# Optimization experiments

Measured on AMD Instinct MI355X. Metric: run time of the kernel, lower is better.

The kernel has to match this reference:

```python
import jax, jax.numpy as jnp
import numpy as np

DIM = 512
HIDDEN = 1024
H2 = HIDDEN // 2
B = 384


def setup_inputs() -> dict:
    key = jax.random.key(0)
    ks = jax.random.split(key, 10)
    s_in = 1.0 / np.sqrt(DIM)
    s_h = 1.0 / np.sqrt(H2)
    return {
        "x_samples": jax.random.normal(ks[0], (B, DIM), dtype=jnp.float32),
        "y_samples": jax.random.normal(ks[1], (B, DIM), dtype=jnp.float32),
        "w1_mu": jax.random.uniform(ks[2], (DIM, H2), jnp.float32, -s_in, s_in),
        "b1_mu": jax.random.uniform(ks[3], (H2,), jnp.float32, -s_in, s_in),
        "w2_mu": jax.random.uniform(ks[4], (H2, DIM), jnp.float32, -s_h, s_h),
        "b2_mu": jax.random.uniform(ks[5], (DIM,), jnp.float32, -s_h, s_h),
        "w1_lv": jax.random.uniform(ks[6], (DIM, H2), jnp.float32, -s_in, s_in),
        "b1_lv": jax.random.uniform(ks[7], (H2,), jnp.float32, -s_in, s_in),
        "w2_lv": jax.random.uniform(ks[8], (H2, DIM), jnp.float32, -s_h, s_h),
        "b2_lv": jax.random.uniform(ks[9], (DIM,), jnp.float32, -s_h, s_h),
    }


def reference(x_samples, y_samples, w1_mu, b1_mu, w2_mu, b2_mu,
              w1_lv, b1_lv, w2_lv, b2_lv):
    batch_size = y_samples.shape[0]
    # p_mu / p_logvar MLPs
    mu = jax.nn.relu(x_samples @ w1_mu + b1_mu) @ w2_mu + b2_mu           # [B, D]
    logvar = jnp.tanh(jax.nn.relu(x_samples @ w1_lv + b1_lv) @ w2_lv + b2_lv)  # [B, D]
    inv_var = jnp.exp(-logvar)

    # positive log-likelihood per sample
    positive = (-(mu - y_samples) ** 2 * 0.5 * inv_var - logvar * 0.5).sum(-1)  # [B]

    # pairwise Gaussian log-likelihoods: all_probs[i, j] = log N(y_j; mu_i)
    diff = y_samples[None, :, :] - mu[:, None, :]                          # [B, B, D]
    all_probs = (-diff ** 2 * 0.5 * inv_var[:, None, :]
                 - logvar[:, None, :] * 0.5).sum(-1)                       # [B, B]

    # faithful to the torch broadcast: [B,B] + [B,B,1] -> [B,B,B]
    diag_mask = jnp.eye(batch_size, dtype=jnp.float32)[:, :, None] * -20.0  # [B, B, 1]
    scores = all_probs + diag_mask                                         # [B, B, B]
    negative = jax.scipy.special.logsumexp(scores, axis=0) - jnp.log(batch_size - 1.0)  # [B, B]

    upper = (positive - negative).mean()

    loglikeli = (-(mu - y_samples) ** 2 * inv_var - logvar).sum(1).mean(0)
    return loglikeli + jax.lax.stop_gradient(-loglikeli + upper)
```

## Files before the change

### kernel.cpp

```cpp
#include <hip/hip_runtime.h>
#include <math.h>

#define NROW 384
#define NCOL 512

#define HP_OFF   0
#define GP_OFF   1572864
#define M1P_OFF  3145728
#define M2P_OFF  3151872
#define M1_OFF   3158016
#define M2_OFF   3158528
#define PART_OFF 3159040
#define CNT_OFF  3159424
#define SLICE    196608

template<int NS>
__device__ __forceinline__ void gemm_block(
    const float* __restrict__ A, const float* __restrict__ bias1,
    const float* __restrict__ W, float* __restrict__ C,
    int m0, int n0, int ca)
{
    __shared__ __align__(16) float As[2][32][36];
    __shared__ __align__(16) float Bs[2][32][68];

    const int t  = threadIdx.x;
    const int tx = t & 15;
    const int ty = t >> 4;
    const int am0 = t >> 3;
    const int ak4 = (t & 7) * 4;
    const int bk  = t >> 4;
    const int bn4 = (t & 15) * 4;

    float4 a_raw[2][NS];
    float4 b_raw[4];
    float4 bias_raw;

    auto load_it = [&](int k0) {
        #pragma unroll
        for (int p = 0; p < 2; ++p) {
            const size_t aoff = (size_t)(m0 + am0 + p * 16) * NCOL + ca + k0 + ak4;
            #pragma unroll
            for (int s = 0; s < NS; ++s)
                a_raw[p][s] = *(const float4*)&A[(size_t)s * SLICE + aoff];
        }
        if (NS > 1) bias_raw = *(const float4*)&bias1[ca + k0 + ak4];
        #pragma unroll
        for (int q = 0; q < 4; ++q)
            b_raw[q] = *(const float4*)&W[(size_t)(ca + k0 + bk + 8 * q) * NCOL + n0 + bn4];
    };

    auto store_it = [&](int buf) {
        #pragma unroll
        for (int p = 0; p < 2; ++p) {
            float v[4];
            if (NS == 1) {
                *(float4*)v = a_raw[p][0];
            } else {
                float s0[4], s1[4], s2[4], s3[4], bb[4];
                *(float4*)s0 = a_raw[p][0]; *(float4*)s1 = a_raw[p][1];
                *(float4*)s2 = a_raw[p][2]; *(float4*)s3 = a_raw[p][3];
                *(float4*)bb = bias_raw;
                #pragma unroll
                for (int j = 0; j < 4; ++j)
                    v[j] = fmaxf(s0[j] + s1[j] + s2[j] + s3[j] + bb[j], 0.f);
            }
            #pragma unroll
            for (int j = 0; j < 4; ++j)
                As[buf][ak4 + j][am0 + p * 16] = v[j];
        }
        #pragma unroll
        for (int q = 0; q < 4; ++q)
            *(float4*)&Bs[buf][bk + 8 * q][bn4] = b_raw[q];
    };

    float acc[4][4] = {};

    load_it(0);
    store_it(0);
    __syncthreads();
    load_it(32);

    for (int it = 0; it < 4; ++it) {
        if (it < 3) {
            store_it((it + 1) & 1);
            if (it < 2) load_it((it + 2) * 32);
        }
        const int buf = it & 1;
        #pragma unroll
        for (int kk = 0; kk < 32; ++kk) {
            float av[4], bv[4];
            *(float4*)av = *(const float4*)&As[buf][kk][ty * 4];
            *(float4*)bv = *(const float4*)&Bs[buf][kk][tx * 4];
            #pragma unroll
            for (int i = 0; i < 4; ++i) {
                acc[i][0] += av[i] * bv[0];
                acc[i][1] += av[i] * bv[1];
                acc[i][2] += av[i] * bv[2];
                acc[i][3] += av[i] * bv[3];
            }
        }
        __syncthreads();
    }

    #pragma unroll
    for (int i = 0; i < 4; ++i)
        *(float4*)&C[(size_t)(m0 + ty * 4 + i) * NCOL + n0 + tx * 4] =
            make_float4(acc[i][0], acc[i][1], acc[i][2], acc[i][3]);
}

__global__ __launch_bounds__(128, 2) void k_layer1(
    const float* __restrict__ x,
    const float* __restrict__ w1mu, const float* __restrict__ w1lv,
    const float* __restrict__ y, float* __restrict__ ws)
{
    const int b = blockIdx.x;
    const int t = threadIdx.x;

    if (b >= 768) {
        const int sb = b - 768;
        const int c  = t * 4;
        float s1[4] = {0.f, 0.f, 0.f, 0.f};
        float s2[4] = {0.f, 0.f, 0.f, 0.f};
        #pragma unroll 4
        for (int r = 0; r < 32; ++r) {
            float v[4];
            *(float4*)v = *(const float4*)&y[(size_t)(sb * 32 + r) * NCOL + c];
            #pragma unroll
            for (int j = 0; j < 4; ++j) { s1[j] += v[j]; s2[j] += v[j] * v[j]; }
        }
        *(float4*)&ws[M1P_OFF + sb * NCOL + c] = make_float4(s1[0], s1[1], s1[2], s1[3]);
        *(float4*)&ws[M2P_OFF + sb * NCOL + c] = make_float4(s2[0], s2[1], s2[2], s2[3]);
        return;
    }

    const int sl   = b & 3;
    const int br   = (b >> 2) & 1;
    const int tile = b >> 3;
    const int mt   = tile >> 3;
    const int nt   = tile & 7;

    gemm_block<1>(x, nullptr, br ? w1lv : w1mu,
                  ws + HP_OFF + (size_t)(br * 4 + sl) * SLICE,
                  mt * 32, nt * 64, sl * 128);
}

__global__ __launch_bounds__(128, 2) void k_layer2(
    const float* __restrict__ b1mu, const float* __restrict__ b1lv,
    const float* __restrict__ w2mu, const float* __restrict__ w2lv,
    float* __restrict__ ws)
{
    const int b = blockIdx.x;
    const int t = threadIdx.x;

    if (b == 768) {
        if (t == 0) *(int*)(ws + CNT_OFF) = 0;
        const int c = t * 4;
        float s1[4] = {0.f, 0.f, 0.f, 0.f};
        float s2[4] = {0.f, 0.f, 0.f, 0.f};
        #pragma unroll
        for (int p = 0; p < 12; ++p) {
            float p1[4], p2[4];
            *(float4*)p1 = *(const float4*)&ws[M1P_OFF + p * NCOL + c];
            *(float4*)p2 = *(const float4*)&ws[M2P_OFF + p * NCOL + c];
            #pragma unroll
            for (int j = 0; j < 4; ++j) { s1[j] += p1[j]; s2[j] += p2[j]; }
        }
        *(float4*)&ws[M1_OFF + c] = make_float4(s1[0], s1[1], s1[2], s1[3]);
        *(float4*)&ws[M2_OFF + c] = make_float4(s2[0], s2[1], s2[2], s2[3]);
        return;
    }

    const int sl   = b & 3;
    const int br   = (b >> 2) & 1;
    const int tile = b >> 3;
    const int mt   = tile >> 3;
    const int nt   = tile & 7;

    gemm_block<4>(ws + HP_OFF + (size_t)(br * 4) * SLICE,
                  br ? b1lv : b1mu, br ? w2lv : w2mu,
                  ws + GP_OFF + (size_t)(br * 4 + sl) * SLICE,
                  mt * 32, nt * 64, sl * 128);
}

__global__ __launch_bounds__(256) void k_epilogue(
    const float* __restrict__ b2mu, const float* __restrict__ b2lv,
    const float* __restrict__ y, float* __restrict__ ws,
    float* __restrict__ out)
{
    __shared__ double wsum[4];
    __shared__ int is_last;

    const int t = threadIdx.x;
    const float inv_b = 1.0f / (float)NROW;

    const int e4   = blockIdx.x * 256 + t;
    const int col4 = e4 & 127;
    const size_t off = (size_t)e4 * 4;

    const float* gpm = ws + GP_OFF;
    const float* gpl = ws + GP_OFF + 4 * SLICE;

    float gm[4] = {0.f, 0.f, 0.f, 0.f};
    float gl[4] = {0.f, 0.f, 0.f, 0.f};
    #pragma unroll
    for (int s = 0; s < 4; ++s) {
        float a[4], c[4];
        *(float4*)a = *(const float4*)&gpm[(size_t)s * SLICE + off];
        *(float4*)c = *(const float4*)&gpl[(size_t)s * SLICE + off];
        #pragma unroll
        for (int j = 0; j < 4; ++j) { gm[j] += a[j]; gl[j] += c[j]; }
    }

    float yv[4], bm[4], bl[4], m1v[4], m2v[4];
    *(float4*)yv  = *(const float4*)&y[off];
    *(float4*)bm  = *(const float4*)&b2mu[col4 * 4];
    *(float4*)bl  = *(const float4*)&b2lv[col4 * 4];
    *(float4*)m1v = *(const float4*)&ws[M1_OFF + col4 * 4];
    *(float4*)m2v = *(const float4*)&ws[M2_OFF + col4 * 4];

    float tsum = 0.f;
    #pragma unroll
    for (int j = 0; j < 4; ++j) {
        const float m1 = m1v[j] * inv_b;
        const float m2 = m2v[j] * inv_b;
        const float mu = gm[j] + bm[j];
        const float lv = tanhf(gl[j] + bl[j]);
        const float iv = expf(-lv);
        tsum += iv * ((yv[j] * yv[j] - m2) + 2.f * mu * (m1 - yv[j]));
    }

    float s = tsum;
    #pragma unroll
    for (int o = 32; o > 0; o >>= 1) s += __shfl_down(s, o);
    if ((t & 63) == 0) wsum[t >> 6] = (double)s;
    __syncthreads();

    double* partials = (double*)(ws + PART_OFF);
    int* counter = (int*)(ws + CNT_OFF);
    if (t == 0) {
        partials[blockIdx.x] = wsum[0] + wsum[1] + wsum[2] + wsum[3];
        __threadfence();
        const int old = atomicAdd(counter, 1);
        is_last = (old == 191) ? 1 : 0;
    }
    __syncthreads();

    if (is_last && t < 64) {
        __threadfence();
        double v = partials[t] + partials[t + 64] + partials[t + 128];
        #pragma unroll
        for (int o = 32; o > 0; o >>= 1) v += __shfl_down(v, o);
        if (t == 0) {
            const double C0 = 5.381602146862063e-12;
            out[0] = (float)(-0.5 * v / (double)NROW - C0);
        }
    }
}

extern "C" void kernel_launch(void* const* d_in, const int* in_sizes, int n_in,
                              void* d_out, int out_size, void* d_ws, size_t ws_size,
                              hipStream_t stream) {
    const float* x    = (const float*)d_in[0];
    const float* y    = (const float*)d_in[1];
    const float* w1mu = (const float*)d_in[2];
    const float* b1mu = (const float*)d_in[3];
    const float* w2mu = (const float*)d_in[4];
    const float* b2mu = (const float*)d_in[5];
    const float* w1lv = (const float*)d_in[6];
    const float* b1lv = (const float*)d_in[7];
    const float* w2lv = (const float*)d_in[8];
    const float* b2lv = (const float*)d_in[9];
    float* out = (float*)d_out;
    float* ws  = (float*)d_ws;

    k_layer1<<<780, 128, 0, stream>>>(x, w1mu, w1lv, y, ws);
    k_layer2<<<769, 128, 0, stream>>>(b1mu, b1lv, w2mu, w2lv, ws);
    k_epilogue<<<192, 256, 0, stream>>>(b2mu, b2lv, y, ws, out);
}
```

Measured before the change: 112.2 us.

## Switch GEMMs to 64x128 tiles with 8-way split-K and 8x8 register blocking

Replaces the 32x64 double-buffered GEMM tile with a single-stage 64x128 tile that covers a 64-deep K chunk, using an 8x8 accumulator per thread and 8 split-K slices instead of 4. Layer-2 now sums 8 partial hidden slices while loading A, and the epilogue reduces 8 output partials. This raises arithmetic intensity per LDS load and halves the block count. In exchange it doubles the partial-sum workspace traffic, drops the load/compute overlap, and uses much more shared memory and registers per block, which may lower occupancy.

```diff
diff --git a/kernel.cpp b/kernel.cpp
--- a/kernel.cpp
+++ b/kernel.cpp
@@ -3,109 +3,94 @@
 
 #define NROW 384
 #define NCOL 512
+#define SLICE 196608
 
 #define HP_OFF   0
-#define GP_OFF   1572864
-#define M1P_OFF  3145728
-#define M2P_OFF  3151872
-#define M1_OFF   3158016
-#define M2_OFF   3158528
-#define PART_OFF 3159040
-#define CNT_OFF  3159424
-#define SLICE    196608
+#define GP_OFF   3145728
+#define M1P_OFF  6291456
+#define M2P_OFF  6297600
+#define M1_OFF   6303744
+#define M2_OFF   6304256
+#define PART_OFF 6304768
+#define CNT_OFF  6305152
 
 template<int NS>
-__device__ __forceinline__ void gemm_block(
+__device__ __forceinline__ void gemm64x128(
     const float* __restrict__ A, const float* __restrict__ bias1,
     const float* __restrict__ W, float* __restrict__ C,
     int m0, int n0, int ca)
 {
-    __shared__ __align__(16) float As[2][32][36];
-    __shared__ __align__(16) float Bs[2][32][68];
-
-    const int t  = threadIdx.x;
-    const int tx = t & 15;
-    const int ty = t >> 4;
-    const int am0 = t >> 3;
-    const int ak4 = (t & 7) * 4;
-    const int bk  = t >> 4;
-    const int bn4 = (t & 15) * 4;
-
-    float4 a_raw[2][NS];
-    float4 b_raw[4];
-    float4 bias_raw;
-
-    auto load_it = [&](int k0) {
-        #pragma unroll
-        for (int p = 0; p < 2; ++p) {
-            const size_t aoff = (size_t)(m0 + am0 + p * 16) * NCOL + ca + k0 + ak4;
-            #pragma unroll
-            for (int s = 0; s < NS; ++s)
-                a_raw[p][s] = *(const float4*)&A[(size_t)s * SLICE + aoff];
-        }
-        if (NS > 1) bias_raw = *(const float4*)&bias1[ca + k0 + ak4];
-        #pragma unroll
-        for (int q = 0; q < 4; ++q)
-            b_raw[q] = *(const float4*)&W[(size_t)(ca + k0 + bk + 8 * q) * NCOL + n0 + bn4];
-    };
-
-    auto store_it = [&](int buf) {
-        #pragma unroll
-        for (int p = 0; p < 2; ++p) {
+    __shared__ __align__(16) float As[64][68];
+    __shared__ __align__(16) float Bs[64][128];
+
+    const int t = threadIdx.x;
+
+    {
+        const int arow  = t & 63;
+        const int ahalf = t >> 6;
+        const float* ap = &A[(size_t)(m0 + arow) * NCOL + ca + ahalf * 32];
+        #pragma unroll
+        for (int g = 0; g < 8; ++g) {
             float v[4];
             if (NS == 1) {
-                *(float4*)v = a_raw[p][0];
+                *(float4*)v = *(const float4*)(ap + g * 4);
             } else {
-                float s0[4], s1[4], s2[4], s3[4], bb[4];
-                *(float4*)s0 = a_raw[p][0]; *(float4*)s1 = a_raw[p][1];
-                *(float4*)s2 = a_raw[p][2]; *(float4*)s3 = a_raw[p][3];
-                *(float4*)bb = bias_raw;
+                float s4[4] = {0.f, 0.f, 0.f, 0.f};
                 #pragma unroll
-                for (int j = 0; j < 4; ++j)
-                    v[j] = fmaxf(s0[j] + s1[j] + s2[j] + s3[j] + bb[j], 0.f);
+                for (int s = 0; s < NS; ++s) {
+                    float u[4];
+                    *(float4*)u = *(const float4*)(ap + (size_t)s * SLICE + g * 4);
+                    s4[0] += u[0]; s4[1] += u[1]; s4[2] += u[2]; s4[3] += u[3];
+                }
+                float bb[4];
+                *(float4*)bb = *(const float4*)&bias1[ca + ahalf * 32 + g * 4];
+                v[0] = fmaxf(s4[0] + bb[0], 0.f);
+                v[1] = fmaxf(s4[1] + bb[1], 0.f);
+                v[2] = fmaxf(s4[2] + bb[2], 0.f);
+                v[3] = fmaxf(s4[3] + bb[3], 0.f);
             }
+            const int k = ahalf * 32 + g * 4;
+            As[k + 0][arow] = v[0];
+            As[k + 1][arow] = v[1];
+            As[k + 2][arow] = v[2];
+            As[k + 3][arow] = v[3];
+        }
+    }
+
+    #pragma unroll
+    for (int i = 0; i < 16; ++i) {
+        const int f4 = t + i * 128;
+        const int kk = f4 >> 5;
+        const int c4 = (f4 & 31) * 4;
+        *(float4*)&Bs[kk][c4] =
+            *(const float4*)&W[(size_t)(ca + kk) * NCOL + n0 + c4];
+    }
+    __syncthreads();
+
+    const int ty = t >> 4, tx = t & 15;
+    float acc[8][8] = {};
+    #pragma unroll 16
+    for (int kk = 0; kk < 64; ++kk) {
+        float a[8], b[8];
+        *(float4*)&a[0] = *(const float4*)&As[kk][ty * 8];
+        *(float4*)&a[4] = *(const float4*)&As[kk][ty * 8 + 4];
+        *(float4*)&b[0] = *(const float4*)&Bs[kk][tx * 4];
+        *(float4*)&b[4] = *(const float4*)&Bs[kk][64 + tx * 4];
+        #pragma unroll
+        for (int i = 0; i < 8; ++i)
             #pragma unroll
-            for (int j = 0; j < 4; ++j)
-                As[buf][ak4 + j][am0 + p * 16] = v[j];
-        }
-        #pragma unroll
-        for (int q = 0; q < 4; ++q)
-            *(float4*)&Bs[buf][bk + 8 * q][bn4] = b_raw[q];
-    };
-
-    float acc[4][4] = {};
-
-    load_it(0);
-    store_it(0);
-    __syncthreads();
-    load_it(32);
-
-    for (int it = 0; it < 4; ++it) {
-        if (it < 3) {
-            store_it((it + 1) & 1);
-            if (it < 2) load_it((it + 2) * 32);
-        }
-        const int buf = it & 1;
-        #pragma unroll
-        for (int kk = 0; kk < 32; ++kk) {
-            float av[4], bv[4];
-            *(float4*)av = *(const float4*)&As[buf][kk][ty * 4];
-            *(float4*)bv = *(const float4*)&Bs[buf][kk][tx * 4];
-            #pragma unroll
-            for (int i = 0; i < 4; ++i) {
-                acc[i][0] += av[i] * bv[0];
-                acc[i][1] += av[i] * bv[1];
-                acc[i][2] += av[i] * bv[2];
-                acc[i][3] += av[i] * bv[3];
-            }
-        }
-        __syncthreads();
-    }
-
-    #pragma unroll
-    for (int i = 0; i < 4; ++i)
-        *(float4*)&C[(size_t)(m0 + ty * 4 + i) * NCOL + n0 + tx * 4] =
+            for (int j = 0; j < 8; ++j)
+                acc[i][j] += a[i] * b[j];
+    }
+
+    #pragma unroll
+    for (int i = 0; i < 8; ++i) {
+        const size_t row = (size_t)(m0 + ty * 8 + i) * NCOL;
+        *(float4*)&C[row + n0 + tx * 4] =
             make_float4(acc[i][0], acc[i][1], acc[i][2], acc[i][3]);
+        *(float4*)&C[row + n0 + 64 + tx * 4] =
+            make_float4(acc[i][4], acc[i][5], acc[i][6], acc[i][7]);
+    }
 }
 
 __global__ __launch_bounds__(128, 2) void k_layer1(
@@ -116,8 +101,8 @@
     const int b = blockIdx.x;
     const int t = threadIdx.x;
 
-    if (b >= 768) {
-        const int sb = b - 768;
+    if (b >= 384) {
+        const int sb = b - 384;
         const int c  = t * 4;
         float s1[4] = {0.f, 0.f, 0.f, 0.f};
         float s2[4] = {0.f, 0.f, 0.f, 0.f};
@@ -133,15 +118,15 @@
         return;
     }
 
-    const int sl   = b & 3;
-    const int br   = (b >> 2) & 1;
-    const int tile = b >> 3;
-    const int mt   = tile >> 3;
-    const int nt   = tile & 7;
-
-    gemm_block<1>(x, nullptr, br ? w1lv : w1mu,
-                  ws + HP_OFF + (size_t)(br * 4 + sl) * SLICE,
-                  mt * 32, nt * 64, sl * 128);
+    const int sl   = b & 7;
+    const int br   = (b >> 3) & 1;
+    const int tile = b >> 4;
+    const int mt   = tile >> 2;
+    const int nt   = tile & 3;
+
+    gemm64x128<1>(x, nullptr, br ? w1lv : w1mu,
+                  ws + HP_OFF + (size_t)(br * 8 + sl) * SLICE,
+                  mt * 64, nt * 128, sl * 64);
 }
 
 __global__ __launch_bounds__(128, 2) void k_layer2(
@@ -152,7 +137,7 @@
     const int b = blockIdx.x;
     const int t = threadIdx.x;
 
-    if (b == 768) {
+    if (b == 384) {
         if (t == 0) *(int*)(ws + CNT_OFF) = 0;
         const int c = t * 4;
         float s1[4] = {0.f, 0.f, 0.f, 0.f};
@@ -170,16 +155,16 @@
         return;
     }
 
-    const int sl   = b & 3;
-    const int br   = (b >> 2) & 1;
-    const int tile = b >> 3;
-    const int mt   = tile >> 3;
-    const int nt   = tile & 7;
-
-    gemm_block<4>(ws + HP_OFF + (size_t)(br * 4) * SLICE,
+    const int sl   = b & 7;
+    const int br   = (b >> 3) & 1;
+    const int tile = b >> 4;
+    const int mt   = tile >> 2;
+    const int nt   = tile & 3;
+
+    gemm64x128<8>(ws + HP_OFF + (size_t)(br * 8) * SLICE,
                   br ? b1lv : b1mu, br ? w2lv : w2mu,
-                  ws + GP_OFF + (size_t)(br * 4 + sl) * SLICE,
-                  mt * 32, nt * 64, sl * 128);
+                  ws + GP_OFF + (size_t)(br * 8 + sl) * SLICE,
+                  mt * 64, nt * 128, sl * 64);
 }
 
 __global__ __launch_bounds__(256) void k_epilogue(
@@ -198,12 +183,12 @@
     const size_t off = (size_t)e4 * 4;
 
     const float* gpm = ws + GP_OFF;
-    const float* gpl = ws + GP_OFF + 4 * SLICE;
+    const float* gpl = ws + GP_OFF + 8 * (size_t)SLICE;
 
     float gm[4] = {0.f, 0.f, 0.f, 0.f};
     float gl[4] = {0.f, 0.f, 0.f, 0.f};
     #pragma unroll
-    for (int s = 0; s < 4; ++s) {
+    for (int s = 0; s < 8; ++s) {
         float a[4], c[4];
         *(float4*)a = *(const float4*)&gpm[(size_t)s * SLICE + off];
         *(float4*)c = *(const float4*)&gpl[(size_t)s * SLICE + off];
@@ -273,7 +258,7 @@
     float* out = (float*)d_out;
     float* ws  = (float*)d_ws;
 
-    k_layer1<<<780, 128, 0, stream>>>(x, w1mu, w1lv, y, ws);
-    k_layer2<<<769, 128, 0, stream>>>(b1mu, b1lv, w2mu, w2lv, ws);
+    k_layer1<<<396, 128, 0, stream>>>(x, w1mu, w1lv, y, ws);
+    k_layer2<<<385, 128, 0, stream>>>(b1mu, b1lv, w2mu, w2lv, ws);
     k_epilogue<<<192, 256, 0, stream>>>(b2mu, b2lv, y, ws, out);
 }
```

Measured after the change: 125.3 us. +11.7%, slower.
